# Performance work log

Hardware: AMD Instinct MI355X
Metric: run time of the kernel (lower is better)

Reference implementation:

```python
import jax, jax.numpy as jnp
import numpy as np
from functools import partial

K_SPARSE = 50  # k_sparse passed as int to __init__
EPS = 1e-12    # numerical guard inside sqrt (diagonal zeros)


def setup_inputs() -> dict:
    key = jax.random.key(0)
    k1, k2, k3, k4 = jax.random.split(key, 4)
    B, n, D = 16, 1000, 128
    locs = jax.random.uniform(k1, (B, n, 2), dtype=jnp.float32)
    init_embeddings = jax.random.normal(k2, (B, n, D), dtype=jnp.float32)
    W = jax.random.normal(k3, (1, D), dtype=jnp.float32) * 0.1  # nn.Linear(1, D).weight.T
    b = jax.random.normal(k4, (D,), dtype=jnp.float32) * 0.1    # nn.Linear bias
    return {"locs": locs, "init_embeddings": init_embeddings, "W": W, "b": b}


def _sparsify(dist):
    """Per-node top-k nearest neighbors (no self loops).
    dist: [B, n, n] -> (neighbor_idx [B, n, k], edge_attr [B, n, k])."""
    B, n, _ = dist.shape
    # mask self loops with +inf so they are never selected
    diag = jnp.eye(n, dtype=bool)
    masked = jnp.where(diag[None, :, :], jnp.inf, dist)
    neg_vals, idx = jax.lax.top_k(-masked, K_SPARSE)  # k smallest distances
    return idx, -neg_vals


def reference(locs, init_embeddings, W, b):
    B, n, _ = locs.shape
    D = init_embeddings.shape[-1]
    k = K_SPARSE

    # pairwise Euclidean distance matrix [B, n, n]
    diff = locs[:, :, None, :] - locs[:, None, :, :]
    dist = jnp.sqrt(jnp.sum(diff * diff, axis=-1) + EPS)

    nbr_idx, edge_attr = _sparsify(dist)  # [B, n, k] each

    # PyG Batch: concatenate graphs with node-index offsets of index * n
    offsets = (jnp.arange(B, dtype=jnp.int32) * n)[:, None]            # [B, 1]
    src = jnp.broadcast_to(jnp.arange(n, dtype=jnp.int32)[:, None], (n, k))
    src = (src.reshape(1, n * k) + offsets).reshape(-1)                # [B*n*k]
    dst = (nbr_idx.reshape(B, n * k).astype(jnp.int32) + offsets).reshape(-1)
    edge_index = jnp.stack([src, dst], axis=0)                          # [2, B*n*k]

    # edge_embed: Linear(1, D) on scalar distances
    edge_emb = edge_attr.reshape(-1, 1) @ W + b                         # [B*n*k, D]

    x = init_embeddings.reshape(B * n, D)                               # batched node feats
    return x, edge_index, edge_emb
```

## Files before the change

### kernel.cpp

```cpp
#include <hip/hip_runtime.h>
#include <cstdint>
#include <cstddef>


namespace {

constexpr int kB  = 16;
constexpr int kN  = 1000;
constexpr int kD  = 128;
constexpr int kK  = 50;
constexpr int kCPL = 16;
constexpr int kNodesPerBlock = 4;
constexpr int kBlocksPerBatch = kN / kNodesPerBlock;

__device__ __forceinline__ double pack_key(float dd, int j) {
  const unsigned long long u =
      ((unsigned long long)__float_as_uint(dd) << 32) | (unsigned)j;
  return __longlong_as_double((long long)u);
}

template<int CTRL>
__device__ __forceinline__ unsigned dpp_min_u32(unsigned x) {
  const unsigned y = (unsigned)__builtin_amdgcn_update_dpp(
      0, (int)x, CTRL, 0xF, 0xF, true);
  return x < y ? x : y;
}

__global__ __launch_bounds__(256)
void tsp_edge_kernel(const float* __restrict__ locs,
                     const float* __restrict__ init_emb,
                     const float* __restrict__ W,
                     const float* __restrict__ bias,
                     float* __restrict__ out)
{
#pragma clang fp contract(off)
  const int tid  = threadIdx.x;
  const int wave = tid >> 6;
  const int lane = tid & 63;
  const int blk  = blockIdx.x;
  const int b    = blk / kBlocksPerBatch;
  const int node_in_b = (blk % kBlocksPerBatch) * kNodesPerBlock + wave;
  const int node = b * kN + node_in_b;

  constexpr size_t X_SZ    = (size_t)kB * kN * kD;
  constexpr size_t E_SZ    = (size_t)kB * kN * kK;
  constexpr size_t SRC_OFF = X_SZ;
  constexpr size_t DST_OFF = X_SZ + E_SZ;
  constexpr size_t EMB_OFF = X_SZ + 2 * E_SZ;

  {
    const float2* srcp = reinterpret_cast<const float2*>(init_emb + (size_t)node * kD);
    float2* dstp = reinterpret_cast<float2*>(out + (size_t)node * kD);
    dstp[lane] = srcp[lane];
  }
  if (lane < kK) {
    out[SRC_OFF + (size_t)node * kK + lane] = (float)node;
  }

  __shared__ __align__(16) float2 sloc[kN];
  {
    const float4* gl4 = reinterpret_cast<const float4*>(locs + (size_t)b * kN * 2);
    float4* sl4 = reinterpret_cast<float4*>(sloc);
    for (int t = tid; t < kN / 2; t += 256) sl4[t] = gl4[t];
  }
  __syncthreads();

  const float2 my = sloc[node_in_b];

  double key[kCPL];
#pragma unroll
  for (int s = 0; s < kCPL; ++s) {
    const int j = lane + (s << 6);
    const bool valid = (j < kN) && (j != node_in_b);
    const float2 pj = sloc[(j < kN) ? j : 0];
    const float dx = my.x - pj.x;
    const float dy = my.y - pj.y;
    const float d2 = dx * dx + dy * dy;
    float dd = sqrtf(d2 + 1e-12f);
    if (!valid) dd = INFINITY;
    key[s] = pack_key(dd, j);
  }

#pragma unroll
  for (int kk = 2; kk <= kCPL; kk <<= 1) {
#pragma unroll
    for (int jj = kk >> 1; jj > 0; jj >>= 1) {
#pragma unroll
      for (int i = 0; i < kCPL; ++i) {
        const int l2 = i ^ jj;
        if (l2 > i) {
          const double a  = key[i];
          const double c  = key[l2];
          const double lo = fmin(a, c);
          const double hi = fmax(a, c);
          if ((i & kk) == 0) { key[i] = lo; key[l2] = hi; }
          else               { key[i] = hi; key[l2] = lo; }
        }
      }
    }
  }

  const float2 wv = reinterpret_cast<const float2*>(W)[lane];
  const float2 bv = reinterpret_cast<const float2*>(bias)[lane];
  float* erow = out + EMB_OFF + (size_t)node * (kK * kD) + lane * 2;

  int res_j = 0;
  const double INFK = __builtin_inf();

#pragma unroll 1
  for (int r = 0; r < kK; ++r) {
    const unsigned long long u0 = (unsigned long long)__double_as_longlong(key[0]);
    const unsigned head_d = (unsigned)(u0 >> 32);
    const unsigned head_j = (unsigned)u0;

    unsigned v = head_d;
    v = dpp_min_u32<0xB1>(v);
    v = dpp_min_u32<0x4E>(v);
    v = dpp_min_u32<0x141>(v);
    v = dpp_min_u32<0x140>(v);
    const unsigned q0 = (unsigned)__builtin_amdgcn_readlane((int)v, 0);
    const unsigned q1 = (unsigned)__builtin_amdgcn_readlane((int)v, 16);
    const unsigned q2 = (unsigned)__builtin_amdgcn_readlane((int)v, 32);
    const unsigned q3 = (unsigned)__builtin_amdgcn_readlane((int)v, 48);
    const unsigned qa = q0 < q1 ? q0 : q1;
    const unsigned qb = q2 < q3 ? q2 : q3;
    const unsigned mu = qa < qb ? qa : qb;

    const unsigned long long msk = __ballot(head_d == mu);
    unsigned jwin = (unsigned)__builtin_amdgcn_readlane(
        (int)head_j, __ffsll((long long)msk) - 1);
    if (__popcll(msk) > 1) {
      unsigned long long mm = msk;
      jwin = 0xFFFFFFFFu;
      while (mm) {
        const int l = __ffsll((long long)mm) - 1;
        const unsigned jj = (unsigned)__builtin_amdgcn_readlane((int)head_j, l);
        jwin = jj < jwin ? jj : jwin;
        mm &= mm - 1;
      }
    }

    if (lane == r) res_j = (int)jwin;

    const float dist = __uint_as_float(mu);
    float2 vv;
    vv.x = dist * wv.x + bv.x;
    vv.y = dist * wv.y + bv.y;
    *reinterpret_cast<float2*>(erow) = vv;
    erow += kD;

    const unsigned long long wk = ((unsigned long long)mu << 32) | jwin;
    const bool pop = (u0 == wk);
#pragma unroll
    for (int s = 0; s < kCPL - 1; ++s) key[s] = pop ? key[s + 1] : key[s];
    key[kCPL - 1] = pop ? INFK : key[kCPL - 1];
  }

  if (lane < kK) {
    out[DST_OFF + (size_t)node * kK + lane] = (float)(b * kN + res_j);
  }
}

}

extern "C" void kernel_launch(void* const* d_in, const int* in_sizes, int n_in,
                              void* d_out, int out_size, void* d_ws, size_t ws_size,
                              hipStream_t stream) {
  const float* locs = (const float*)d_in[0];
  const float* emb  = (const float*)d_in[1];
  const float* W    = (const float*)d_in[2];
  const float* bias = (const float*)d_in[3];
  float* out = (float*)d_out;

  dim3 grid(kB * kBlocksPerBatch);
  dim3 block(256);
  hipLaunchKernelGGL(tsp_edge_kernel, grid, block, 0, stream, locs, emb, W, bias, out);
}
```

Baseline: 445.6 us.

## Split top-k selection and edge-embedding expansion into two kernels via workspace

Selection now writes the k nearest distances per node to a workspace buffer instead of emitting the 128-wide edge embedding rows inside the serial 50-step extraction loop. A second grid-stride kernel expands the distances into the embedding with float4 stores, keeping the memory system busy independently of the selection latency. The fused kernel is kept as a fallback when no workspace is available. The cost is an extra launch and a small round trip through the buffer, and the benefit depends on the workspace being provided.

Result: slower. 507.7 us (+13.9%).

```diff
diff --git a/kernel.cpp b/kernel.cpp
--- a/kernel.cpp
+++ b/kernel.cpp
@@ -13,6 +13,13 @@
 constexpr int kNodesPerBlock = 4;
 constexpr int kBlocksPerBatch = kN / kNodesPerBlock;
 
+constexpr size_t X_SZ    = (size_t)kB * kN * kD;
+constexpr size_t E_SZ    = (size_t)kB * kN * kK;
+constexpr size_t SRC_OFF = X_SZ;
+constexpr size_t DST_OFF = X_SZ + E_SZ;
+constexpr size_t EMB_OFF = X_SZ + 2 * E_SZ;
+constexpr size_t EMB_F4  = (E_SZ * kD) / 4;
+
 __device__ __forceinline__ double pack_key(float dd, int j) {
   const unsigned long long u =
       ((unsigned long long)__float_as_uint(dd) << 32) | (unsigned)j;
@@ -27,11 +34,10 @@
 }
 
 __global__ __launch_bounds__(256)
-void tsp_edge_kernel(const float* __restrict__ locs,
-                     const float* __restrict__ init_emb,
-                     const float* __restrict__ W,
-                     const float* __restrict__ bias,
-                     float* __restrict__ out)
+void tsp_select_kernel(const float* __restrict__ locs,
+                       const float* __restrict__ init_emb,
+                       float* __restrict__ out,
+                       float* __restrict__ dbuf)
 {
 #pragma clang fp contract(off)
   const int tid  = threadIdx.x;
@@ -41,12 +47,6 @@
   const int b    = blk / kBlocksPerBatch;
   const int node_in_b = (blk % kBlocksPerBatch) * kNodesPerBlock + wave;
   const int node = b * kN + node_in_b;
-
-  constexpr size_t X_SZ    = (size_t)kB * kN * kD;
-  constexpr size_t E_SZ    = (size_t)kB * kN * kK;
-  constexpr size_t SRC_OFF = X_SZ;
-  constexpr size_t DST_OFF = X_SZ + E_SZ;
-  constexpr size_t EMB_OFF = X_SZ + 2 * E_SZ;
 
   {
     const float2* srcp = reinterpret_cast<const float2*>(init_emb + (size_t)node * kD);
@@ -100,11 +100,8 @@
     }
   }
 
-  const float2 wv = reinterpret_cast<const float2*>(W)[lane];
-  const float2 bv = reinterpret_cast<const float2*>(bias)[lane];
-  float* erow = out + EMB_OFF + (size_t)node * (kK * kD) + lane * 2;
-
-  int res_j = 0;
+  float res_d = 0.0f;
+  int   res_j = 0;
   const double INFK = __builtin_inf();
 
 #pragma unroll 1
@@ -140,6 +137,155 @@
       }
     }
 
+    if (lane == r) { res_j = (int)jwin; res_d = __uint_as_float(mu); }
+
+    const unsigned long long wk = ((unsigned long long)mu << 32) | jwin;
+    const bool pop = (u0 == wk);
+#pragma unroll
+    for (int s = 0; s < kCPL - 1; ++s) key[s] = pop ? key[s + 1] : key[s];
+    key[kCPL - 1] = pop ? INFK : key[kCPL - 1];
+  }
+
+  if (lane < kK) {
+    dbuf[(size_t)node * kK + lane] = res_d;
+    out[DST_OFF + (size_t)node * kK + lane] = (float)(b * kN + res_j);
+  }
+}
+
+__global__ __launch_bounds__(256)
+void tsp_expand_kernel(const float* __restrict__ dbuf,
+                       const float* __restrict__ W,
+                       const float* __restrict__ bias,
+                       float* __restrict__ out)
+{
+#pragma clang fp contract(off)
+  const size_t g      = (size_t)blockIdx.x * blockDim.x + threadIdx.x;
+  const size_t stride = (size_t)gridDim.x * blockDim.x;
+
+  const int c4 = (int)(g & 31);
+  const float4 w4 = reinterpret_cast<const float4*>(W)[c4];
+  const float4 b4 = reinterpret_cast<const float4*>(bias)[c4];
+  float4* eout = reinterpret_cast<float4*>(out + EMB_OFF);
+
+  for (size_t i = g; i < EMB_F4; i += stride) {
+    const float dist = dbuf[i >> 5];
+    float4 v;
+    v.x = dist * w4.x + b4.x;
+    v.y = dist * w4.y + b4.y;
+    v.z = dist * w4.z + b4.z;
+    v.w = dist * w4.w + b4.w;
+    eout[i] = v;
+  }
+}
+
+__global__ __launch_bounds__(256)
+void tsp_edge_fused(const float* __restrict__ locs,
+                    const float* __restrict__ init_emb,
+                    const float* __restrict__ W,
+                    const float* __restrict__ bias,
+                    float* __restrict__ out)
+{
+#pragma clang fp contract(off)
+  const int tid  = threadIdx.x;
+  const int wave = tid >> 6;
+  const int lane = tid & 63;
+  const int blk  = blockIdx.x;
+  const int b    = blk / kBlocksPerBatch;
+  const int node_in_b = (blk % kBlocksPerBatch) * kNodesPerBlock + wave;
+  const int node = b * kN + node_in_b;
+
+  {
+    const float2* srcp = reinterpret_cast<const float2*>(init_emb + (size_t)node * kD);
+    float2* dstp = reinterpret_cast<float2*>(out + (size_t)node * kD);
+    dstp[lane] = srcp[lane];
+  }
+  if (lane < kK) {
+    out[SRC_OFF + (size_t)node * kK + lane] = (float)node;
+  }
+
+  __shared__ __align__(16) float2 sloc[kN];
+  {
+    const float4* gl4 = reinterpret_cast<const float4*>(locs + (size_t)b * kN * 2);
+    float4* sl4 = reinterpret_cast<float4*>(sloc);
+    for (int t = tid; t < kN / 2; t += 256) sl4[t] = gl4[t];
+  }
+  __syncthreads();
+
+  const float2 my = sloc[node_in_b];
+
+  double key[kCPL];
+#pragma unroll
+  for (int s = 0; s < kCPL; ++s) {
+    const int j = lane + (s << 6);
+    const bool valid = (j < kN) && (j != node_in_b);
+    const float2 pj = sloc[(j < kN) ? j : 0];
+    const float dx = my.x - pj.x;
+    const float dy = my.y - pj.y;
+    const float d2 = dx * dx + dy * dy;
+    float dd = sqrtf(d2 + 1e-12f);
+    if (!valid) dd = INFINITY;
+    key[s] = pack_key(dd, j);
+  }
+
+#pragma unroll
+  for (int kk = 2; kk <= kCPL; kk <<= 1) {
+#pragma unroll
+    for (int jj = kk >> 1; jj > 0; jj >>= 1) {
+#pragma unroll
+      for (int i = 0; i < kCPL; ++i) {
+        const int l2 = i ^ jj;
+        if (l2 > i) {
+          const double a  = key[i];
+          const double c  = key[l2];
+          const double lo = fmin(a, c);
+          const double hi = fmax(a, c);
+          if ((i & kk) == 0) { key[i] = lo; key[l2] = hi; }
+          else               { key[i] = hi; key[l2] = lo; }
+        }
+      }
+    }
+  }
+
+  const float2 wv = reinterpret_cast<const float2*>(W)[lane];
+  const float2 bv = reinterpret_cast<const float2*>(bias)[lane];
+  float* erow = out + EMB_OFF + (size_t)node * (kK * kD) + lane * 2;
+
+  int res_j = 0;
+  const double INFK = __builtin_inf();
+
+#pragma unroll 1
+  for (int r = 0; r < kK; ++r) {
+    const unsigned long long u0 = (unsigned long long)__double_as_longlong(key[0]);
+    const unsigned head_d = (unsigned)(u0 >> 32);
+    const unsigned head_j = (unsigned)u0;
+
+    unsigned v = head_d;
+    v = dpp_min_u32<0xB1>(v);
+    v = dpp_min_u32<0x4E>(v);
+    v = dpp_min_u32<0x141>(v);
+    v = dpp_min_u32<0x140>(v);
+    const unsigned q0 = (unsigned)__builtin_amdgcn_readlane((int)v, 0);
+    const unsigned q1 = (unsigned)__builtin_amdgcn_readlane((int)v, 16);
+    const unsigned q2 = (unsigned)__builtin_amdgcn_readlane((int)v, 32);
+    const unsigned q3 = (unsigned)__builtin_amdgcn_readlane((int)v, 48);
+    const unsigned qa = q0 < q1 ? q0 : q1;
+    const unsigned qb = q2 < q3 ? q2 : q3;
+    const unsigned mu = qa < qb ? qa : qb;
+
+    const unsigned long long msk = __ballot(head_d == mu);
+    unsigned jwin = (unsigned)__builtin_amdgcn_readlane(
+        (int)head_j, __ffsll((long long)msk) - 1);
+    if (__popcll(msk) > 1) {
+      unsigned long long mm = msk;
+      jwin = 0xFFFFFFFFu;
+      while (mm) {
+        const int l = __ffsll((long long)mm) - 1;
+        const unsigned jj = (unsigned)__builtin_amdgcn_readlane((int)head_j, l);
+        jwin = jj < jwin ? jj : jwin;
+        mm &= mm - 1;
+      }
+    }
+
     if (lane == r) res_j = (int)jwin;
 
     const float dist = __uint_as_float(mu);
@@ -172,7 +318,21 @@
   const float* bias = (const float*)d_in[3];
   float* out = (float*)d_out;
 
-  dim3 grid(kB * kBlocksPerBatch);
-  dim3 block(256);
-  hipLaunchKernelGGL(tsp_edge_kernel, grid, block, 0, stream, locs, emb, W, bias, out);
-}
+  const size_t need = (size_t)kB * kN * kK * sizeof(float);
+
+  if (d_ws != nullptr && ws_size >= need) {
+    float* dbuf = (float*)d_ws;
+    dim3 grid1(kB * kBlocksPerBatch);
+    dim3 block(256);
+    hipLaunchKernelGGL(tsp_select_kernel, grid1, block, 0, stream,
+                       locs, emb, out, dbuf);
+    dim3 grid2(2048);
+    hipLaunchKernelGGL(tsp_expand_kernel, grid2, block, 0, stream,
+                       dbuf, W, bias, out);
+  } else {
+    dim3 grid(kB * kBlocksPerBatch);
+    dim3 block(256);
+    hipLaunchKernelGGL(tsp_edge_fused, grid, block, 0, stream,
+                       locs, emb, W, bias, out);
+  }
+}
```
